# Performance work log

Hardware: AMD Instinct MI355X
Metric: run time of the kernel (lower is better)

Reference implementation:

```python
import jax, jax.numpy as jnp
import numpy as np

KERNEL_SIZE = 15  # module init kwarg


def _box_filter(x, k):
    c = x.shape[1]
    dn = ('NCHW', 'OIHW', 'NCHW')
    kh = jnp.ones((c, 1, k, 1), x.dtype)
    kw = jnp.ones((c, 1, 1, k), x.dtype)
    p = k // 2
    x = jax.lax.conv_general_dilated(x, kh, (1, 1), [(p, p), (0, 0)],
                                     dimension_numbers=dn, feature_group_count=c)
    x = jax.lax.conv_general_dilated(x, kw, (1, 1), [(0, 0), (p, p)],
                                     dimension_numbers=dn, feature_group_count=c)
    return x


def setup_inputs() -> dict:
    key = jax.random.key(0)
    k1, k2 = jax.random.split(key)
    b, c, h, w = 8, 19, 512, 1024
    input = jax.random.normal(k1, (b, c, h, w), dtype=jnp.float32)
    target = jax.random.randint(k2, (b, 1, h, w), 0, c, dtype=jnp.int32)
    return {"input": input, "target": target}


def reference(input, target):
    k = KERNEL_SIZE
    c = input.shape[1]
    # one-hot mask [b,c,h,w] (equivalent to the per-class (target==i) cat loop)
    mask = jnp.transpose(jax.nn.one_hot(target[:, 0], c, dtype=input.dtype), (0, 3, 1, 2))
    # per-class local count of same-class pixels in a k x k window
    count = _box_filter(mask, k)
    # since mask is one-hot, sum over channels picks the count at the true class (>= 1)
    wsum = jnp.sum(count * mask, axis=1, keepdims=True)  # [b,1,h,w]
    weight = (k * k) / wsum
    # gather the input score at the true class and weight it
    out = jnp.sum(input * mask, axis=1, keepdims=True) * (-weight)
    return jnp.mean(out)
```

## Files before the change

### kernel.cpp

```cpp
#include <hip/hip_runtime.h>
#include <stdint.h>

#define BB 8
#define CC 19
#define HH 512
#define WW 1024
#define KK 15
#define RR 7
#define TH 8
#define NROWS (TH + 2*RR)
#define ROW_DW 260
#define NPIX (BB*HH*WW)
#define SENT4 0x1F1F1F1Fu

static __device__ __forceinline__ uint32_t alignb(uint32_t hi, uint32_t lo, unsigned s) {
#if __has_builtin(__builtin_amdgcn_alignbyte)
  return __builtin_amdgcn_alignbyte(hi, lo, s);
#else
  return (uint32_t)(((((uint64_t)hi) << 32) | lo) >> (8u * s));
#endif
}

__global__ __launch_bounds__(256) void wce_main(const float* __restrict__ in,
                                                const int* __restrict__ tg,
                                                float* __restrict__ part) {
  __shared__ uint32_t T[NROWS][ROW_DW];
  __shared__ float wpart[4];
  const int tid = threadIdx.x;
  const int blk = blockIdx.x;
  const int bb  = blk >> 6;
  const int h0  = (blk & 63) * TH;

  const int total = NROWS * ROW_DW;
  for (int idx = tid; idx < total; idx += 256) {
    const int r = idx / ROW_DW;
    const int d = idx - r * ROW_DW;
    uint32_t v = SENT4;
    const int h = h0 - RR + r;
    if (h >= 0 && h < HH && d >= 2 && d < 258) {
      const int4 t4 = *reinterpret_cast<const int4*>(&tg[(bb*HH + h)*WW + (d - 2)*4]);
      v = (uint32_t)(t4.x & 0xff)        | ((uint32_t)(t4.y & 0xff) << 8)
        | ((uint32_t)(t4.z & 0xff) << 16) | ((uint32_t)(t4.w & 0xff) << 24);
    }
    (&T[0][0])[idx] = v;
  }
  __syncthreads();

  const int g = tid;
  float acc = 0.0f;

  #pragma unroll 1
  for (int s = 0; s < TH; ++s) {
    const int hh = h0 + s;
    const uint32_t c4 = T[s + RR][g + 2];

    const int c0 = (int)(c4 & 0xff), c1 = (int)((c4 >> 8) & 0xff);
    const int c2 = (int)((c4 >> 16) & 0xff), c3 = (int)((c4 >> 24) & 0xff);
    const int base = bb*CC*HH*WW + hh*WW + 4*g;
    const float x0 = in[base + c0*(HH*WW) + 0];
    const float x1 = in[base + c1*(HH*WW) + 1];
    const float x2 = in[base + c2*(HH*WW) + 2];
    const float x3 = in[base + c3*(HH*WW) + 3];

    uint32_t nm = 0;
    #pragma unroll
    for (int wr = 0; wr < KK; ++wr) {
      const uint32_t* row = &T[s + wr][g];
      const uint32_t d0 = row[0], d1 = row[1], d2 = row[2], d3 = row[3], d4 = row[4];
      #define CMPW(rhs) do { uint32_t t_ = ((rhs) ^ c4) + 0x7f7f7f7fu; \
                             nm += (t_ & 0x80808080u) >> 7; } while (0)
      CMPW(alignb(d1, d0, 1));
      CMPW(alignb(d1, d0, 2));
      CMPW(alignb(d1, d0, 3));
      CMPW(d1);
      CMPW(alignb(d2, d1, 1));
      CMPW(alignb(d2, d1, 2));
      CMPW(alignb(d2, d1, 3));
      CMPW(d2);
      CMPW(alignb(d3, d2, 1));
      CMPW(alignb(d3, d2, 2));
      CMPW(alignb(d3, d2, 3));
      CMPW(d3);
      CMPW(alignb(d4, d3, 1));
      CMPW(alignb(d4, d3, 2));
      CMPW(alignb(d4, d3, 3));
      #undef CMPW
    }
    const int n0 = 225 - (int)( nm        & 0xff);
    const int n1 = 225 - (int)((nm >> 8)  & 0xff);
    const int n2 = 225 - (int)((nm >> 16) & 0xff);
    const int n3 = 225 - (int)((nm >> 24) & 0xff);
    acc += x0 * (225.0f / (float)n0);
    acc += x1 * (225.0f / (float)n1);
    acc += x2 * (225.0f / (float)n2);
    acc += x3 * (225.0f / (float)n3);
  }

  #pragma unroll
  for (int off = 32; off > 0; off >>= 1) acc += __shfl_down(acc, off, 64);
  const int lane = tid & 63, wv = tid >> 6;
  if (lane == 0) wpart[wv] = acc;
  __syncthreads();
  if (tid == 0) part[blk] = wpart[0] + wpart[1] + wpart[2] + wpart[3];
}

__global__ __launch_bounds__(256) void wce_reduce(const float* __restrict__ part,
                                                  float* __restrict__ out, int n) {
  __shared__ float wpart[4];
  float a = 0.0f;
  for (int i = threadIdx.x; i < n; i += 256) a += part[i];
  #pragma unroll
  for (int off = 32; off > 0; off >>= 1) a += __shfl_down(a, off, 64);
  const int lane = threadIdx.x & 63, wv = threadIdx.x >> 6;
  if (lane == 0) wpart[wv] = a;
  __syncthreads();
  if (threadIdx.x == 0) {
    const float tot = wpart[0] + wpart[1] + wpart[2] + wpart[3];
    out[0] = -tot / (float)NPIX;
  }
}

extern "C" void kernel_launch(void* const* d_in, const int* in_sizes, int n_in,
                              void* d_out, int out_size, void* d_ws, size_t ws_size,
                              hipStream_t stream) {
  const float* in = (const float*)d_in[0];
  const int*   tg = (const int*)d_in[1];
  float* out  = (float*)d_out;
  float* part = (float*)d_ws;

  const int nblk = BB * (HH / TH);
  wce_main<<<nblk, 256, 0, stream>>>(in, tg, part);
  wce_reduce<<<1, 256, 0, stream>>>(part, out, nblk);
}
```

Measured before the change: 56.07 us.

## Halve rows per block and prefetch next row's gathered inputs with nontemporal loads

Each block now covers 4 output rows instead of 8, doubling the grid to 1024 blocks. The scattered input gathers for row s+1 are issued before the window-count work of row s, so their latency overlaps the ALU compare loop. The loads use nontemporal hints because the data is read once. Fewer rows per block means the 14 halo rows loaded into shared memory are amortised over less output, which raises shared-memory fill work per output pixel.

```diff
diff --git a/kernel.cpp b/kernel.cpp
--- a/kernel.cpp
+++ b/kernel.cpp
@@ -7,10 +7,11 @@
 #define WW 1024
 #define KK 15
 #define RR 7
-#define TH 8
+#define TH 4
 #define NROWS (TH + 2*RR)
 #define ROW_DW 260
 #define NPIX (BB*HH*WW)
+#define HW (HH*WW)
 #define SENT4 0x1F1F1F1Fu
 
 static __device__ __forceinline__ uint32_t alignb(uint32_t hi, uint32_t lo, unsigned s) {
@@ -28,8 +29,8 @@
   __shared__ float wpart[4];
   const int tid = threadIdx.x;
   const int blk = blockIdx.x;
-  const int bb  = blk >> 6;
-  const int h0  = (blk & 63) * TH;
+  const int bb  = blk >> 7;
+  const int h0  = (blk & 127) * TH;
 
   const int total = NROWS * ROW_DW;
   for (int idx = tid; idx < total; idx += 256) {
@@ -49,18 +50,28 @@
   const int g = tid;
   float acc = 0.0f;
 
+  uint32_t c4 = T[RR][g + 2];
+  float x0, x1, x2, x3;
+  {
+    const int base = bb*CC*HW + h0*WW + 4*g;
+    x0 = __builtin_nontemporal_load(&in[base + (int)( c4        & 0xff)*HW + 0]);
+    x1 = __builtin_nontemporal_load(&in[base + (int)((c4 >> 8)  & 0xff)*HW + 1]);
+    x2 = __builtin_nontemporal_load(&in[base + (int)((c4 >> 16) & 0xff)*HW + 2]);
+    x3 = __builtin_nontemporal_load(&in[base + (int)((c4 >> 24) & 0xff)*HW + 3]);
+  }
+
   #pragma unroll 1
   for (int s = 0; s < TH; ++s) {
-    const int hh = h0 + s;
-    const uint32_t c4 = T[s + RR][g + 2];
-
-    const int c0 = (int)(c4 & 0xff), c1 = (int)((c4 >> 8) & 0xff);
-    const int c2 = (int)((c4 >> 16) & 0xff), c3 = (int)((c4 >> 24) & 0xff);
-    const int base = bb*CC*HH*WW + hh*WW + 4*g;
-    const float x0 = in[base + c0*(HH*WW) + 0];
-    const float x1 = in[base + c1*(HH*WW) + 1];
-    const float x2 = in[base + c2*(HH*WW) + 2];
-    const float x3 = in[base + c3*(HH*WW) + 3];
+    uint32_t c4n = 0;
+    float y0 = 0.f, y1 = 0.f, y2 = 0.f, y3 = 0.f;
+    if (s + 1 < TH) {
+      c4n = T[s + 1 + RR][g + 2];
+      const int base = bb*CC*HW + (h0 + s + 1)*WW + 4*g;
+      y0 = __builtin_nontemporal_load(&in[base + (int)( c4n        & 0xff)*HW + 0]);
+      y1 = __builtin_nontemporal_load(&in[base + (int)((c4n >> 8)  & 0xff)*HW + 1]);
+      y2 = __builtin_nontemporal_load(&in[base + (int)((c4n >> 16) & 0xff)*HW + 2]);
+      y3 = __builtin_nontemporal_load(&in[base + (int)((c4n >> 24) & 0xff)*HW + 3]);
+    }
 
     uint32_t nm = 0;
     #pragma unroll
@@ -94,6 +105,8 @@
     acc += x1 * (225.0f / (float)n1);
     acc += x2 * (225.0f / (float)n2);
     acc += x3 * (225.0f / (float)n3);
+
+    x0 = y0; x1 = y1; x2 = y2; x3 = y3; c4 = c4n;
   }
 
   #pragma unroll
```

Measured after the change: 66.97 us. +19.4%, slower.

## Software-pipeline gathers across rows and fuse final reduction via atomic last-block

Applied to the files above, without the earlier changes.

The row loop is unrolled by two and the scattered input gather for the next row is issued before the 15x15 window compare of the current row, so global load latency overlaps with the ALU-heavy count. The separate reduce kernel is removed: each block atomically adds its partial sum and a counter, and the last block writes the mean. A memset of the workspace is added per launch. This adds atomic contention, non-deterministic float summation order, and an extra memset node, while saving one kernel launch.

```diff
diff --git a/kernel.cpp b/kernel.cpp
--- a/kernel.cpp
+++ b/kernel.cpp
@@ -11,6 +11,8 @@
 #define NROWS (TH + 2*RR)
 #define ROW_DW 260
 #define NPIX (BB*HH*WW)
+#define HW (HH*WW)
+#define NBLK (BB*(HH/TH))
 #define SENT4 0x1F1F1F1Fu
 
 static __device__ __forceinline__ uint32_t alignb(uint32_t hi, uint32_t lo, unsigned s) {
@@ -23,7 +25,8 @@
 
 __global__ __launch_bounds__(256) void wce_main(const float* __restrict__ in,
                                                 const int* __restrict__ tg,
-                                                float* __restrict__ part) {
+                                                float* __restrict__ wsF,
+                                                float* __restrict__ out) {
   __shared__ uint32_t T[NROWS][ROW_DW];
   __shared__ float wpart[4];
   const int tid = threadIdx.x;
@@ -47,76 +50,78 @@
   __syncthreads();
 
   const int g = tid;
+  const int gbase = bb*CC*HW + h0*WW + 4*g;
   float acc = 0.0f;
 
+  #define WINDOW(s_, c4_, x0_, x1_, x2_, x3_) do {                              \
+    uint32_t nm = 0;                                                            \
+    _Pragma("unroll")                                                           \
+    for (int wr = 0; wr < KK; ++wr) {                                           \
+      const uint32_t* row = &T[(s_) + wr][g];                                   \
+      const uint32_t d0 = row[0], d1 = row[1], d2 = row[2], d3 = row[3], d4 = row[4]; \
+      uint32_t t_;                                                              \
+      t_ = (alignb(d1, d0, 1) ^ (c4_)) + 0x7f7f7f7fu; nm += (t_ & 0x80808080u) >> 7; \
+      t_ = (alignb(d1, d0, 2) ^ (c4_)) + 0x7f7f7f7fu; nm += (t_ & 0x80808080u) >> 7; \
+      t_ = (alignb(d1, d0, 3) ^ (c4_)) + 0x7f7f7f7fu; nm += (t_ & 0x80808080u) >> 7; \
+      t_ = (d1              ^ (c4_)) + 0x7f7f7f7fu; nm += (t_ & 0x80808080u) >> 7; \
+      t_ = (alignb(d2, d1, 1) ^ (c4_)) + 0x7f7f7f7fu; nm += (t_ & 0x80808080u) >> 7; \
+      t_ = (alignb(d2, d1, 2) ^ (c4_)) + 0x7f7f7f7fu; nm += (t_ & 0x80808080u) >> 7; \
+      t_ = (alignb(d2, d1, 3) ^ (c4_)) + 0x7f7f7f7fu; nm += (t_ & 0x80808080u) >> 7; \
+      t_ = (d2              ^ (c4_)) + 0x7f7f7f7fu; nm += (t_ & 0x80808080u) >> 7; \
+      t_ = (alignb(d3, d2, 1) ^ (c4_)) + 0x7f7f7f7fu; nm += (t_ & 0x80808080u) >> 7; \
+      t_ = (alignb(d3, d2, 2) ^ (c4_)) + 0x7f7f7f7fu; nm += (t_ & 0x80808080u) >> 7; \
+      t_ = (alignb(d3, d2, 3) ^ (c4_)) + 0x7f7f7f7fu; nm += (t_ & 0x80808080u) >> 7; \
+      t_ = (d3              ^ (c4_)) + 0x7f7f7f7fu; nm += (t_ & 0x80808080u) >> 7; \
+      t_ = (alignb(d4, d3, 1) ^ (c4_)) + 0x7f7f7f7fu; nm += (t_ & 0x80808080u) >> 7; \
+      t_ = (alignb(d4, d3, 2) ^ (c4_)) + 0x7f7f7f7fu; nm += (t_ & 0x80808080u) >> 7; \
+      t_ = (alignb(d4, d3, 3) ^ (c4_)) + 0x7f7f7f7fu; nm += (t_ & 0x80808080u) >> 7; \
+    }                                                                           \
+    acc += (x0_) * (225.0f / (float)(225 - (int)( nm        & 0xff)));          \
+    acc += (x1_) * (225.0f / (float)(225 - (int)((nm >> 8)  & 0xff)));          \
+    acc += (x2_) * (225.0f / (float)(225 - (int)((nm >> 16) & 0xff)));          \
+    acc += (x3_) * (225.0f / (float)(225 - (int)((nm >> 24) & 0xff)));          \
+  } while (0)
+
+  #define GATHER(s_, c4_, x0_, x1_, x2_, x3_) do {                              \
+    (c4_) = T[(s_) + RR][g + 2];                                                \
+    const int b_ = gbase + (s_)*WW;                                             \
+    (x0_) = in[b_ + (int)( (c4_)        & 0xff)*HW + 0];                        \
+    (x1_) = in[b_ + (int)(((c4_) >> 8)  & 0xff)*HW + 1];                        \
+    (x2_) = in[b_ + (int)(((c4_) >> 16) & 0xff)*HW + 2];                        \
+    (x3_) = in[b_ + (int)(((c4_) >> 24) & 0xff)*HW + 3];                        \
+  } while (0)
+
+  uint32_t c4a, c4b;
+  float a0, a1, a2, a3, b0, b1, b2, b3;
+  GATHER(0, c4a, a0, a1, a2, a3);
+
   #pragma unroll 1
-  for (int s = 0; s < TH; ++s) {
-    const int hh = h0 + s;
-    const uint32_t c4 = T[s + RR][g + 2];
-
-    const int c0 = (int)(c4 & 0xff), c1 = (int)((c4 >> 8) & 0xff);
-    const int c2 = (int)((c4 >> 16) & 0xff), c3 = (int)((c4 >> 24) & 0xff);
-    const int base = bb*CC*HH*WW + hh*WW + 4*g;
-    const float x0 = in[base + c0*(HH*WW) + 0];
-    const float x1 = in[base + c1*(HH*WW) + 1];
-    const float x2 = in[base + c2*(HH*WW) + 2];
-    const float x3 = in[base + c3*(HH*WW) + 3];
-
-    uint32_t nm = 0;
-    #pragma unroll
-    for (int wr = 0; wr < KK; ++wr) {
-      const uint32_t* row = &T[s + wr][g];
-      const uint32_t d0 = row[0], d1 = row[1], d2 = row[2], d3 = row[3], d4 = row[4];
-      #define CMPW(rhs) do { uint32_t t_ = ((rhs) ^ c4) + 0x7f7f7f7fu; \
-                             nm += (t_ & 0x80808080u) >> 7; } while (0)
-      CMPW(alignb(d1, d0, 1));
-      CMPW(alignb(d1, d0, 2));
-      CMPW(alignb(d1, d0, 3));
-      CMPW(d1);
-      CMPW(alignb(d2, d1, 1));
-      CMPW(alignb(d2, d1, 2));
-      CMPW(alignb(d2, d1, 3));
-      CMPW(d2);
-      CMPW(alignb(d3, d2, 1));
-      CMPW(alignb(d3, d2, 2));
-      CMPW(alignb(d3, d2, 3));
-      CMPW(d3);
-      CMPW(alignb(d4, d3, 1));
-      CMPW(alignb(d4, d3, 2));
-      CMPW(alignb(d4, d3, 3));
-      #undef CMPW
-    }
-    const int n0 = 225 - (int)( nm        & 0xff);
-    const int n1 = 225 - (int)((nm >> 8)  & 0xff);
-    const int n2 = 225 - (int)((nm >> 16) & 0xff);
-    const int n3 = 225 - (int)((nm >> 24) & 0xff);
-    acc += x0 * (225.0f / (float)n0);
-    acc += x1 * (225.0f / (float)n1);
-    acc += x2 * (225.0f / (float)n2);
-    acc += x3 * (225.0f / (float)n3);
+  for (int s = 0; s < TH; s += 2) {
+    GATHER(s + 1, c4b, b0, b1, b2, b3);
+    WINDOW(s, c4a, a0, a1, a2, a3);
+    const int s2 = (s + 2 < TH) ? s + 2 : s;
+    GATHER(s2, c4a, a0, a1, a2, a3);
+    WINDOW(s + 1, c4b, b0, b1, b2, b3);
   }
+  #undef GATHER
+  #undef WINDOW
 
   #pragma unroll
   for (int off = 32; off > 0; off >>= 1) acc += __shfl_down(acc, off, 64);
   const int lane = tid & 63, wv = tid >> 6;
   if (lane == 0) wpart[wv] = acc;
   __syncthreads();
-  if (tid == 0) part[blk] = wpart[0] + wpart[1] + wpart[2] + wpart[3];
-}
 
-__global__ __launch_bounds__(256) void wce_reduce(const float* __restrict__ part,
-                                                  float* __restrict__ out, int n) {
-  __shared__ float wpart[4];
-  float a = 0.0f;
-  for (int i = threadIdx.x; i < n; i += 256) a += part[i];
-  #pragma unroll
-  for (int off = 32; off > 0; off >>= 1) a += __shfl_down(a, off, 64);
-  const int lane = threadIdx.x & 63, wv = threadIdx.x >> 6;
-  if (lane == 0) wpart[wv] = a;
-  __syncthreads();
-  if (threadIdx.x == 0) {
-    const float tot = wpart[0] + wpart[1] + wpart[2] + wpart[3];
-    out[0] = -tot / (float)NPIX;
+  if (tid == 0) {
+    const float bsum = wpart[0] + wpart[1] + wpart[2] + wpart[3];
+    atomicAdd(&wsF[0], bsum);
+    __threadfence();
+    const int old = atomicAdd((int*)&wsF[1], 1);
+    if (old == NBLK - 1) {
+      __threadfence();
+      const float tot = __hip_atomic_load(&wsF[0], __ATOMIC_RELAXED, __HIP_MEMORY_SCOPE_AGENT);
+      out[0] = -tot / (float)NPIX;
+    }
   }
 }
 
@@ -125,10 +130,9 @@
                               hipStream_t stream) {
   const float* in = (const float*)d_in[0];
   const int*   tg = (const int*)d_in[1];
-  float* out  = (float*)d_out;
-  float* part = (float*)d_ws;
+  float* out = (float*)d_out;
+  float* ws  = (float*)d_ws;
 
-  const int nblk = BB * (HH / TH);
-  wce_main<<<nblk, 256, 0, stream>>>(in, tg, part);
-  wce_reduce<<<1, 256, 0, stream>>>(part, out, nblk);
+  hipMemsetAsync(d_ws, 0, 8, stream);
+  wce_main<<<NBLK, 256, 0, stream>>>(in, tg, ws, out);
 }
```

New measurement: 81.06 us. +44.6%, slower.

## Replace SWAR byte comparisons with per-class bitplanes and popcount window counts

Applied to the files above, without the earlier changes.

Shared memory now holds one bitmask plane per class instead of the packed byte labels. The planes are built with LDS atomicOr, and each pixel's same-class count comes from 15 funnel-shift plus popcount operations on its own class plane. This replaces the 225 byte-wise compare/accumulate steps per 4-pixel group and is meant to cut ALU work in the inner window loop. In exchange it adds a zeroing pass over about 52KB of LDS, atomic contention while building the planes, and larger LDS use that can lower occupancy. Each pixel's plane reads also depend on its class, so the LDS accesses may hit bank conflicts.

```diff
diff --git a/kernel.cpp b/kernel.cpp
--- a/kernel.cpp
+++ b/kernel.cpp
@@ -9,40 +9,43 @@
 #define RR 7
 #define TH 8
 #define NROWS (TH + 2*RR)
-#define ROW_DW 260
+#define P_DW 34
 #define NPIX (BB*HH*WW)
-#define SENT4 0x1F1F1F1Fu
-
-static __device__ __forceinline__ uint32_t alignb(uint32_t hi, uint32_t lo, unsigned s) {
-#if __has_builtin(__builtin_amdgcn_alignbyte)
-  return __builtin_amdgcn_alignbyte(hi, lo, s);
-#else
-  return (uint32_t)(((((uint64_t)hi) << 32) | lo) >> (8u * s));
-#endif
-}
+#define NBLK (BB*(HH/TH))
 
 __global__ __launch_bounds__(256) void wce_main(const float* __restrict__ in,
                                                 const int* __restrict__ tg,
                                                 float* __restrict__ part) {
-  __shared__ uint32_t T[NROWS][ROW_DW];
+  __shared__ uint32_t P[CC][NROWS][P_DW];
+  __shared__ uint32_t Cc[TH][256];
   __shared__ float wpart[4];
   const int tid = threadIdx.x;
   const int blk = blockIdx.x;
   const int bb  = blk >> 6;
   const int h0  = (blk & 63) * TH;
 
-  const int total = NROWS * ROW_DW;
-  for (int idx = tid; idx < total; idx += 256) {
-    const int r = idx / ROW_DW;
-    const int d = idx - r * ROW_DW;
-    uint32_t v = SENT4;
+  uint32_t* pflat = &P[0][0][0];
+  #pragma unroll 4
+  for (int i = tid; i < CC*NROWS*P_DW; i += 256) pflat[i] = 0;
+  __syncthreads();
+
+  for (int idx = tid; idx < NROWS*256; idx += 256) {
+    const int r = idx >> 8, d = idx & 255;
     const int h = h0 - RR + r;
-    if (h >= 0 && h < HH && d >= 2 && d < 258) {
-      const int4 t4 = *reinterpret_cast<const int4*>(&tg[(bb*HH + h)*WW + (d - 2)*4]);
-      v = (uint32_t)(t4.x & 0xff)        | ((uint32_t)(t4.y & 0xff) << 8)
-        | ((uint32_t)(t4.z & 0xff) << 16) | ((uint32_t)(t4.w & 0xff) << 24);
+    if (h >= 0 && h < HH) {
+      const int4 t4 = *reinterpret_cast<const int4*>(&tg[(bb*HH + h)*WW + d*4]);
+      const int rc = r - RR;
+      if (rc >= 0 && rc < TH)
+        Cc[rc][d] = (uint32_t)(t4.x & 0xff)        | ((uint32_t)(t4.y & 0xff) << 8)
+                  | ((uint32_t)(t4.z & 0xff) << 16) | ((uint32_t)(t4.w & 0xff) << 24);
+      const int col = d * 4;
+      const int dw  = 1 + (col >> 5);
+      const int b   = col & 31;
+      atomicOr(&P[t4.x][r][dw], 1u << (b + 0));
+      atomicOr(&P[t4.y][r][dw], 1u << (b + 1));
+      atomicOr(&P[t4.z][r][dw], 1u << (b + 2));
+      atomicOr(&P[t4.w][r][dw], 1u << (b + 3));
     }
-    (&T[0][0])[idx] = v;
   }
   __syncthreads();
 
@@ -51,49 +54,37 @@
 
   #pragma unroll 1
   for (int s = 0; s < TH; ++s) {
-    const int hh = h0 + s;
-    const uint32_t c4 = T[s + RR][g + 2];
+    const uint32_t c4 = Cc[s][g];
 
     const int c0 = (int)(c4 & 0xff), c1 = (int)((c4 >> 8) & 0xff);
     const int c2 = (int)((c4 >> 16) & 0xff), c3 = (int)((c4 >> 24) & 0xff);
-    const int base = bb*CC*HH*WW + hh*WW + 4*g;
+    const int base = bb*CC*HH*WW + (h0 + s)*WW + 4*g;
     const float x0 = in[base + c0*(HH*WW) + 0];
     const float x1 = in[base + c1*(HH*WW) + 1];
     const float x2 = in[base + c2*(HH*WW) + 2];
     const float x3 = in[base + c3*(HH*WW) + 3];
 
-    uint32_t nm = 0;
+    int cnt[4];
     #pragma unroll
-    for (int wr = 0; wr < KK; ++wr) {
-      const uint32_t* row = &T[s + wr][g];
-      const uint32_t d0 = row[0], d1 = row[1], d2 = row[2], d3 = row[3], d4 = row[4];
-      #define CMPW(rhs) do { uint32_t t_ = ((rhs) ^ c4) + 0x7f7f7f7fu; \
-                             nm += (t_ & 0x80808080u) >> 7; } while (0)
-      CMPW(alignb(d1, d0, 1));
-      CMPW(alignb(d1, d0, 2));
-      CMPW(alignb(d1, d0, 3));
-      CMPW(d1);
-      CMPW(alignb(d2, d1, 1));
-      CMPW(alignb(d2, d1, 2));
-      CMPW(alignb(d2, d1, 3));
-      CMPW(d2);
-      CMPW(alignb(d3, d2, 1));
-      CMPW(alignb(d3, d2, 2));
-      CMPW(alignb(d3, d2, 3));
-      CMPW(d3);
-      CMPW(alignb(d4, d3, 1));
-      CMPW(alignb(d4, d3, 2));
-      CMPW(alignb(d4, d3, 3));
-      #undef CMPW
+    for (int i = 0; i < 4; ++i) {
+      const int c  = (int)((c4 >> (8*i)) & 0xff);
+      const int lb = 4*g + i - 7;
+      const int q  = (lb >> 5) + 1;
+      const int sh = lb & 31;
+      const uint32_t* pr = &P[c][s][q];
+      int cn = 0;
+      #pragma unroll
+      for (int wr = 0; wr < KK; ++wr) {
+        const uint32_t lo = pr[0], hi = pr[1];
+        cn += __popc(__builtin_amdgcn_alignbit(hi, lo, sh) & 0x7fffu);
+        pr += P_DW;
+      }
+      cnt[i] = cn;
     }
-    const int n0 = 225 - (int)( nm        & 0xff);
-    const int n1 = 225 - (int)((nm >> 8)  & 0xff);
-    const int n2 = 225 - (int)((nm >> 16) & 0xff);
-    const int n3 = 225 - (int)((nm >> 24) & 0xff);
-    acc += x0 * (225.0f / (float)n0);
-    acc += x1 * (225.0f / (float)n1);
-    acc += x2 * (225.0f / (float)n2);
-    acc += x3 * (225.0f / (float)n3);
+    acc += x0 * (225.0f / (float)cnt[0]);
+    acc += x1 * (225.0f / (float)cnt[1]);
+    acc += x2 * (225.0f / (float)cnt[2]);
+    acc += x3 * (225.0f / (float)cnt[3]);
   }
 
   #pragma unroll
@@ -128,7 +119,6 @@
   float* out  = (float*)d_out;
   float* part = (float*)d_ws;
 
-  const int nblk = BB * (HH / TH);
-  wce_main<<<nblk, 256, 0, stream>>>(in, tg, part);
-  wce_reduce<<<1, 256, 0, stream>>>(part, out, nblk);
+  wce_main<<<NBLK, 256, 0, stream>>>(in, tg, part);
+  wce_reduce<<<1, 256, 0, stream>>>(part, out, NBLK);
 }
```

New measurement: 53.87 us. 1.04x faster.
